# Performance work log

Hardware: AMD Instinct MI355X
Metric: run time of the kernel (lower is better)

The kernel has to match this reference:

```python
import jax, jax.numpy as jnp
import numpy as np

IMAGE_SIZE = (256, 704)
VOXEL_SIZE = (0.5, 0.5, 1.5)
N_VOXELS = (200, 200, 4)
VOXEL_CENTER = (0.0, 0.0, -1.7)
BN_EPS = 1e-5
B, N_CAM, C_IN, HF, WF, C_OUT = 2, 6, 256, 32, 88, 80


def _get_points():
    nx, ny, nz = N_VOXELS
    pts = jnp.stack(jnp.meshgrid(jnp.arange(nx), jnp.arange(ny), jnp.arange(nz), indexing='ij')).astype(jnp.float32)
    vs = jnp.asarray(VOXEL_SIZE, jnp.float32)
    origin = jnp.asarray(VOXEL_CENTER, jnp.float32) - jnp.asarray(N_VOXELS, jnp.float32) / 2.0 * vs
    pts = pts * vs.reshape(3, 1, 1, 1) + origin.reshape(3, 1, 1, 1)
    return pts.reshape(3, -1)  # [3, N], N = nx*ny*nz


def setup_inputs():
    key = jax.random.key(0)
    k0, k1 = jax.random.split(key)
    mlvl_feats = jax.random.normal(k0, (B, N_CAM, C_IN, HF, WF), jnp.float32)
    # realistic lidar2image = intrinsics @ extrinsics for 6 surround cameras
    H, W = IMAGE_SIZE
    K = np.eye(4, dtype=np.float32)
    K[0, 0], K[1, 1], K[0, 2], K[1, 2] = 350.0, 350.0, W / 2.0, H / 2.0
    l2i = np.zeros((B, N_CAM, 4, 4), np.float32)
    A = np.array([[0, -1, 0], [0, 0, -1], [1, 0, 0]], np.float32)  # lidar->camera axis remap
    for j in range(N_CAM):
        yaw = 2.0 * np.pi * j / N_CAM
        cz, sz = np.cos(yaw), np.sin(yaw)
        Rz = np.array([[cz, -sz, 0], [sz, cz, 0], [0, 0, 1]], np.float32)
        R = A @ Rz.T
        t = Rz @ np.array([1.0, 0.0, 1.5], np.float32)  # camera position in lidar frame
        E = np.eye(4, dtype=np.float32)
        E[:3, :3] = R
        E[:3, 3] = -R @ t
        l2i[:, j] = K @ E
    lidar2image = jnp.asarray(l2i)
    img_aug_matrix = jnp.tile(jnp.eye(4, dtype=jnp.float32), (B, N_CAM, 1, 1))
    lidar_aug_matrix = jnp.tile(jnp.eye(4, dtype=jnp.float32), (B, 1, 1))
    conv_w = jax.random.normal(k1, (C_OUT, C_IN), jnp.float32) * 0.05
    conv_b = jnp.zeros((C_OUT,), jnp.float32)
    bn_gamma = jnp.ones((C_OUT,), jnp.float32)
    bn_beta = jnp.zeros((C_OUT,), jnp.float32)
    bn_mean = jnp.zeros((C_OUT,), jnp.float32)
    bn_var = jnp.ones((C_OUT,), jnp.float32)
    return {"mlvl_feats": mlvl_feats, "lidar2image": lidar2image, "img_aug_matrix": img_aug_matrix,
            "lidar_aug_matrix": lidar_aug_matrix, "conv_w": conv_w, "conv_b": conv_b,
            "bn_gamma": bn_gamma, "bn_beta": bn_beta, "bn_mean": bn_mean, "bn_var": bn_var}


def _sample_volume(feat, l2i, iam, lam, pts):
    # feat: [n_cam, C, Hf, Wf]; l2i/iam: [n_cam,4,4]; lam: [4,4]; pts: [3,N]
    n_img, C, Hh, Ww = feat.shape
    stride = (IMAGE_SIZE[-1] + Ww - 1) // Ww  # ceil(image_W / feat_W)
    p = pts - lam[:3, 3:4]
    p = lam[:3, :3].T @ p  # inverse lidar aug
    iam_r = iam.at[:, :3, 3].set(0.0)  # img aug with translation zeroed
    proj = (iam_r @ l2i)[:, :3, :]  # [n_cam, 3, 4]
    ph = jnp.concatenate([p, jnp.ones((1, p.shape[1]), p.dtype)], axis=0)  # [4, N]
    p2i = jnp.einsum('nij,jk->nik', proj, ph)  # [n_cam, 3, N]
    Z = p2i[:, 2]
    u = p2i[:, 0] / Z + iam[:, 0, 3][:, None]
    v = p2i[:, 1] / Z + iam[:, 1, 3][:, None]
    u_fm = jnp.round(u / stride).astype(jnp.int32)
    v_fm = jnp.round(v / stride).astype(jnp.int32)
    valid = (u_fm >= 0) & (v_fm >= 0) & (u_fm < Ww) & (v_fm < Hh) & (Z > 0)
    uc = jnp.clip(u_fm, 0, Ww - 1)
    vc = jnp.clip(v_fm, 0, Hh - 1)
    vol = jnp.zeros((C, pts.shape[1]), feat.dtype)
    for j in range(n_img):  # fixed small camera count; later cameras overwrite, matching torch loop
        vol = jnp.where(valid[j][None, :], feat[j][:, vc[j], uc[j]], vol)
    return vol.reshape(C, *N_VOXELS).sum(axis=-1)  # sum over z -> [C, nx, ny]


def reference(mlvl_feats, lidar2image, img_aug_matrix, lidar_aug_matrix, conv_w, conv_b, bn_gamma, bn_beta, bn_mean, bn_var):
    pts = _get_points()
    bev = jax.vmap(_sample_volume, in_axes=(0, 0, 0, 0, None))(
        mlvl_feats, lidar2image, img_aug_matrix, lidar_aug_matrix, pts)  # [B, C, nx, ny]
    out = jnp.einsum('bcxy,oc->boxy', bev, conv_w) + conv_b[None, :, None, None]
    scale = (bn_gamma / jnp.sqrt(bn_var + BN_EPS))[None, :, None, None]
    out = (out - bn_mean[None, :, None, None]) * scale + bn_beta[None, :, None, None]
    return jnp.maximum(out, 0.0)
```

## Files before the change

### kernel.cpp

```cpp
#include <hip/hip_runtime.h>
#include <hip/hip_fp16.h>

#define BATCH 2
#define NCAM 6
#define CIN 256
#define COUT 80
#define HFEAT 32
#define WFEAT 88
#define HWF (HFEAT * WFEAT)
#define NXV 200
#define NYV 200
#define NZV 4
#define NPIX (NXV * NYV)
#define BN_EPS 1e-5f
#define CSPLIT 2
#define CHALF (COUT / CSPLIT)

#define NTILE 132
#define NTILE_PAD 136
#define FEATW_BLOCKS 544

#define WS_NEED ((size_t)BATCH * NCAM * HWF * COUT * 2)

__device__ __forceinline__ void compute_cam_mat(int b, int cam,
                                                const float* __restrict__ l2i,
                                                const float* __restrict__ iam,
                                                const float* __restrict__ lam,
                                                float* __restrict__ O ) {
    const float* L = lam + b * 16;
    const float* A = iam + (b * NCAM + cam) * 16;
    const float* P = l2i + (b * NCAM + cam) * 16;
    float Tl[3][4];
    #pragma unroll
    for (int i = 0; i < 3; i++) {
        #pragma unroll
        for (int j = 0; j < 3; j++) Tl[i][j] = L[j * 4 + i];
        Tl[i][3] = -(L[0 * 4 + i] * L[0 * 4 + 3] +
                     L[1 * 4 + i] * L[1 * 4 + 3] +
                     L[2 * 4 + i] * L[2 * 4 + 3]);
    }
    float Pm[3][4];
    #pragma unroll
    for (int i = 0; i < 3; i++)
        #pragma unroll
        for (int j = 0; j < 4; j++) {
            float s = 0.f;
            #pragma unroll
            for (int k = 0; k < 3; k++) s += A[i * 4 + k] * P[k * 4 + j];
            Pm[i][j] = s;
        }
    #pragma unroll
    for (int i = 0; i < 3; i++) {
        #pragma unroll
        for (int j = 0; j < 4; j++) {
            float s = (j == 3) ? Pm[i][3] : 0.f;
            #pragma unroll
            for (int k = 0; k < 3; k++) s += Pm[i][k] * Tl[k][j];
            O[i * 4 + j] = s;
        }
    }
    O[12] = A[0 * 4 + 3];
    O[13] = A[1 * 4 + 3];
    O[14] = 0.f;
    O[15] = 0.f;
}

__global__ __launch_bounds__(256) void k_featw(const float* __restrict__ feat,
                                               const float* __restrict__ W,
                                               __half* __restrict__ featW) {
    __shared__ __align__(16) float wl[CIN][20];
    const int id = blockIdx.x;
    const int r = id & 7;
    const int s = id >> 3;
    const int q = s % 17;
    const int og = s / 17;
    const int T = q * 8 + r;
    if (T >= NTILE) return;
    const int bc = T / 11;
    const int xt = T % 11;
    const int l = threadIdx.x;

    #pragma unroll
    for (int j = 0; j < 20; j++)
        wl[l][j] = W[(og * 20 + j) * CIN + l];
    __syncthreads();

    const int hw = xt * 256 + l;
    const float* f = feat + (size_t)bc * CIN * HWF + hw;

    float acc[20];
    #pragma unroll
    for (int j = 0; j < 20; j++) acc[j] = 0.f;

    float fbA[16], fbB[16];
    #pragma unroll
    for (int k = 0; k < 16; k++) fbA[k] = f[(size_t)k * HWF];

    #pragma unroll
    for (int cc = 0; cc < CIN; cc += 32) {
        #pragma unroll
        for (int k = 0; k < 16; k++) fbB[k] = f[(size_t)(cc + 16 + k) * HWF];
        #pragma unroll
        for (int k = 0; k < 16; k++) {
            float v = fbA[k];
            const float4* wr = reinterpret_cast<const float4*>(&wl[cc + k][0]);
            float4 w0 = wr[0], w1 = wr[1], w2 = wr[2], w3 = wr[3], w4 = wr[4];
            acc[0]  = fmaf(v, w0.x, acc[0]);   acc[1]  = fmaf(v, w0.y, acc[1]);
            acc[2]  = fmaf(v, w0.z, acc[2]);   acc[3]  = fmaf(v, w0.w, acc[3]);
            acc[4]  = fmaf(v, w1.x, acc[4]);   acc[5]  = fmaf(v, w1.y, acc[5]);
            acc[6]  = fmaf(v, w1.z, acc[6]);   acc[7]  = fmaf(v, w1.w, acc[7]);
            acc[8]  = fmaf(v, w2.x, acc[8]);   acc[9]  = fmaf(v, w2.y, acc[9]);
            acc[10] = fmaf(v, w2.z, acc[10]);  acc[11] = fmaf(v, w2.w, acc[11]);
            acc[12] = fmaf(v, w3.x, acc[12]);  acc[13] = fmaf(v, w3.y, acc[13]);
            acc[14] = fmaf(v, w3.z, acc[14]);  acc[15] = fmaf(v, w3.w, acc[15]);
            acc[16] = fmaf(v, w4.x, acc[16]);  acc[17] = fmaf(v, w4.y, acc[17]);
            acc[18] = fmaf(v, w4.z, acc[18]);  acc[19] = fmaf(v, w4.w, acc[19]);
        }
        if (cc + 32 < CIN) {
            #pragma unroll
            for (int k = 0; k < 16; k++) fbA[k] = f[(size_t)(cc + 32 + k) * HWF];
        }
        #pragma unroll
        for (int k = 0; k < 16; k++) {
            float v = fbB[k];
            const float4* wr = reinterpret_cast<const float4*>(&wl[cc + 16 + k][0]);
            float4 w0 = wr[0], w1 = wr[1], w2 = wr[2], w3 = wr[3], w4 = wr[4];
            acc[0]  = fmaf(v, w0.x, acc[0]);   acc[1]  = fmaf(v, w0.y, acc[1]);
            acc[2]  = fmaf(v, w0.z, acc[2]);   acc[3]  = fmaf(v, w0.w, acc[3]);
            acc[4]  = fmaf(v, w1.x, acc[4]);   acc[5]  = fmaf(v, w1.y, acc[5]);
            acc[6]  = fmaf(v, w1.z, acc[6]);   acc[7]  = fmaf(v, w1.w, acc[7]);
            acc[8]  = fmaf(v, w2.x, acc[8]);   acc[9]  = fmaf(v, w2.y, acc[9]);
            acc[10] = fmaf(v, w2.z, acc[10]);  acc[11] = fmaf(v, w2.w, acc[11]);
            acc[12] = fmaf(v, w3.x, acc[12]);  acc[13] = fmaf(v, w3.y, acc[13]);
            acc[14] = fmaf(v, w3.z, acc[14]);  acc[15] = fmaf(v, w3.w, acc[15]);
            acc[16] = fmaf(v, w4.x, acc[16]);  acc[17] = fmaf(v, w4.y, acc[17]);
            acc[18] = fmaf(v, w4.z, acc[18]);  acc[19] = fmaf(v, w4.w, acc[19]);
        }
    }

    __half2* dst = reinterpret_cast<__half2*>(
        featW + ((size_t)bc * HWF + hw) * COUT + og * 20);
    #pragma unroll
    for (int j = 0; j < 10; j++)
        dst[j] = __floats2half2_rn(acc[2 * j], acc[2 * j + 1]);
}

__device__ __forceinline__ int project_point(const float* __restrict__ M ,
                                             float x, float y, float z) {
    for (int cam = NCAM - 1; cam >= 0; --cam) {
        const float* m = M + cam * 16;
        float Z = m[8] * x + m[9] * y + m[10] * z + m[11];
        if (Z > 0.f) {
            float u = (m[0] * x + m[1] * y + m[2] * z + m[3]) / Z + m[12];
            float v = (m[4] * x + m[5] * y + m[6] * z + m[7]) / Z + m[13];
            float uf = rintf(u * 0.125f);
            float vf = rintf(v * 0.125f);
            if (uf >= 0.f && uf < (float)WFEAT && vf >= 0.f && vf < (float)HFEAT) {
                return cam * HWF + (int)vf * WFEAT + (int)uf;
            }
        }
    }
    return -1;
}

__device__ __forceinline__ void bn_precompute(const float* __restrict__ cb,
                                              const float* __restrict__ gamma,
                                              const float* __restrict__ beta,
                                              const float* __restrict__ mean,
                                              const float* __restrict__ var,
                                              float* __restrict__ s_scale,
                                              float* __restrict__ s_bias) {
    for (int o = threadIdx.x; o < COUT; o += 64) {
        float sc = gamma[o] / sqrtf(var[o] + BN_EPS);
        s_scale[o] = sc;
        s_bias[o] = (cb[o] - mean[o]) * sc + beta[o];
    }
}

__global__ __launch_bounds__(64) void k_bev(const __half* __restrict__ featW,
                                            const float* __restrict__ l2i,
                                            const float* __restrict__ iam,
                                            const float* __restrict__ lam,
                                            const float* __restrict__ cb,
                                            const float* __restrict__ gamma,
                                            const float* __restrict__ beta,
                                            const float* __restrict__ mean,
                                            const float* __restrict__ var,
                                            float* __restrict__ out) {
    __shared__ float smats[NCAM * 16];
    __shared__ float s_scale[COUT];
    __shared__ float s_bias[COUT];
    const int b = blockIdx.y;
    const int cs = blockIdx.z;
    if (threadIdx.x < NCAM)
        compute_cam_mat(b, threadIdx.x, l2i, iam, lam, smats + threadIdx.x * 16);
    bn_precompute(cb, gamma, beta, mean, var, s_scale, s_bias);
    __syncthreads();

    const int P = blockIdx.x * 64 + threadIdx.x;
    const int ix = P / NYV, iy = P % NYV;
    const float x = ix * 0.5f - 50.0f;
    const float y = iy * 0.5f - 50.0f;

    const __half* base = featW + (size_t)b * NCAM * HWF * COUT + cs * CHALF;
    const uint4* src[NZV];
    float vmask[NZV];
    #pragma unroll
    for (int iz = 0; iz < NZV; ++iz) {
        float z = iz * 1.5f - 4.7f;
        int off = project_point(smats, x, y, z);
        vmask[iz] = (off >= 0) ? 1.0f : 0.0f;
        src[iz] = reinterpret_cast<const uint4*>(
            base + (size_t)((off >= 0) ? off : 0) * COUT);
    }

    uint4 buf[NZV][5];
    #pragma unroll
    for (int iz = 0; iz < NZV; ++iz)
        #pragma unroll
        for (int i = 0; i < 5; i++) buf[iz][i] = src[iz][i];

    float acc[CHALF];
    #pragma unroll
    for (int k = 0; k < CHALF; k++) acc[k] = 0.f;
    #pragma unroll
    for (int iz = 0; iz < NZV; ++iz) {
        float m = vmask[iz];
        #pragma unroll
        for (int i = 0; i < 5; i++) {
            const __half2* h2 = reinterpret_cast<const __half2*>(&buf[iz][i]);
            #pragma unroll
            for (int k = 0; k < 4; k++) {
                float2 fv = __half22float2(h2[k]);
                acc[i * 8 + k * 2]     = fmaf(m, fv.x, acc[i * 8 + k * 2]);
                acc[i * 8 + k * 2 + 1] = fmaf(m, fv.y, acc[i * 8 + k * 2 + 1]);
            }
        }
    }

    float* op = out + ((size_t)b * COUT + cs * CHALF) * NPIX + P;
    #pragma unroll
    for (int k = 0; k < CHALF; k++) {
        int o = cs * CHALF + k;
        float val = fmaf(acc[k], s_scale[o], s_bias[o]);
        op[(size_t)k * NPIX] = fmaxf(val, 0.f);
    }
}

__global__ __launch_bounds__(64) void k_bev_fb(const float* __restrict__ feat,
                                               const float* __restrict__ l2i,
                                               const float* __restrict__ iam,
                                               const float* __restrict__ lam,
                                               const float* __restrict__ W,
                                               const float* __restrict__ cb,
                                               const float* __restrict__ gamma,
                                               const float* __restrict__ beta,
                                               const float* __restrict__ mean,
                                               const float* __restrict__ var,
                                               float* __restrict__ out) {
    __shared__ float smats[NCAM * 16];
    __shared__ float s_scale[COUT];
    __shared__ float s_bias[COUT];
    const int b = blockIdx.y;
    if (threadIdx.x < NCAM)
        compute_cam_mat(b, threadIdx.x, l2i, iam, lam, smats + threadIdx.x * 16);
    bn_precompute(cb, gamma, beta, mean, var, s_scale, s_bias);
    __syncthreads();

    const int P = blockIdx.x * 64 + threadIdx.x;
    const int ix = P / NYV, iy = P % NYV;
    const float x = ix * 0.5f - 50.0f;
    const float y = iy * 0.5f - 50.0f;

    float acc[COUT];
    #pragma unroll
    for (int o = 0; o < COUT; o++) acc[o] = 0.f;

    for (int iz = 0; iz < NZV; ++iz) {
        float z = iz * 1.5f - 4.7f;
        int off = project_point(smats, x, y, z);
        if (off >= 0) {
            const float* fp = feat + (size_t)b * NCAM * CIN * HWF +
                              (size_t)(off / HWF) * CIN * HWF + (off % HWF);
            for (int c = 0; c < CIN; c++) {
                float fv = fp[(size_t)c * HWF];
                #pragma unroll 8
                for (int o = 0; o < COUT; o++) acc[o] = fmaf(fv, W[o * CIN + c], acc[o]);
            }
        }
    }

    float* op = out + (size_t)b * COUT * NPIX + P;
    for (int o = 0; o < COUT; o++) {
        float val = fmaf(acc[o], s_scale[o], s_bias[o]);
        op[(size_t)o * NPIX] = fmaxf(val, 0.f);
    }
}

extern "C" void kernel_launch(void* const* d_in, const int* in_sizes, int n_in,
                              void* d_out, int out_size, void* d_ws, size_t ws_size,
                              hipStream_t stream) {
    const float* feat  = (const float*)d_in[0];
    const float* l2i   = (const float*)d_in[1];
    const float* iam   = (const float*)d_in[2];
    const float* lam   = (const float*)d_in[3];
    const float* W     = (const float*)d_in[4];
    const float* cb    = (const float*)d_in[5];
    const float* gamma = (const float*)d_in[6];
    const float* beta  = (const float*)d_in[7];
    const float* mean  = (const float*)d_in[8];
    const float* var   = (const float*)d_in[9];
    float* out = (float*)d_out;

    if (ws_size >= WS_NEED) {
        __half* featWp = (__half*)d_ws;
        k_featw<<<FEATW_BLOCKS, 256, 0, stream>>>(feat, W, featWp);
        k_bev<<<dim3(625, 2, CSPLIT), 64, 0, stream>>>(featWp, l2i, iam, lam, cb,
                                                       gamma, beta, mean, var, out);
    } else {
        k_bev_fb<<<dim3(625, 2), 64, 0, stream>>>(feat, l2i, iam, lam, W, cb, gamma,
                                                  beta, mean, var, out);
    }
}
```

Before: 134.0 us.

## Register-block four pixels per thread in feature-weight GEMM with 64-thread blocks

The projection GEMM kernel now runs 64 threads per block, and each thread computes four pixels (strided by 64) across 20 output channels. Each weight value read from shared memory is reused four times, cutting LDS traffic per FMA, and the feature prefetch depth is halved to 8 channels. The cost is many more live registers (80 accumulators plus 64 buffered features) and fewer waves per block, which may lower occupancy and latency hiding on the global loads.

New measurement: 292.2 us. 2.18x slower.

```diff
diff --git a/kernel.cpp b/kernel.cpp
--- a/kernel.cpp
+++ b/kernel.cpp
@@ -17,7 +17,6 @@
 #define CHALF (COUT / CSPLIT)
 
 #define NTILE 132
-#define NTILE_PAD 136
 #define FEATW_BLOCKS 544
 
 #define WS_NEED ((size_t)BATCH * NCAM * HWF * COUT * 2)
@@ -65,9 +64,9 @@
     O[15] = 0.f;
 }
 
-__global__ __launch_bounds__(256) void k_featw(const float* __restrict__ feat,
-                                               const float* __restrict__ W,
-                                               __half* __restrict__ featW) {
+__global__ __launch_bounds__(64, 2) void k_featw(const float* __restrict__ feat,
+                                                 const float* __restrict__ W,
+                                                 __half* __restrict__ featW) {
     __shared__ __align__(16) float wl[CIN][20];
     const int id = blockIdx.x;
     const int r = id & 7;
@@ -81,68 +80,81 @@
     const int l = threadIdx.x;
 
     #pragma unroll
+    for (int j = 0; j < 20; j++) {
+        #pragma unroll
+        for (int qq = 0; qq < 4; qq++) {
+            int c = qq * 64 + l;
+            wl[c][j] = W[(og * 20 + j) * CIN + c];
+        }
+    }
+    __syncthreads();
+
+    const int hw0 = xt * 256;
+    const float* f = feat + (size_t)bc * CIN * HWF + hw0 + l;
+
+    float acc[20][4];
+    #pragma unroll
     for (int j = 0; j < 20; j++)
-        wl[l][j] = W[(og * 20 + j) * CIN + l];
-    __syncthreads();
-
-    const int hw = xt * 256 + l;
-    const float* f = feat + (size_t)bc * CIN * HWF + hw;
-
-    float acc[20];
-    #pragma unroll
-    for (int j = 0; j < 20; j++) acc[j] = 0.f;
-
-    float fbA[16], fbB[16];
-    #pragma unroll
-    for (int k = 0; k < 16; k++) fbA[k] = f[(size_t)k * HWF];
-
-    #pragma unroll
-    for (int cc = 0; cc < CIN; cc += 32) {
-        #pragma unroll
-        for (int k = 0; k < 16; k++) fbB[k] = f[(size_t)(cc + 16 + k) * HWF];
-        #pragma unroll
-        for (int k = 0; k < 16; k++) {
-            float v = fbA[k];
+        #pragma unroll
+        for (int p = 0; p < 4; p++) acc[j][p] = 0.f;
+
+    float fbA[8][4], fbB[8][4];
+    #pragma unroll
+    for (int k = 0; k < 8; k++)
+        #pragma unroll
+        for (int p = 0; p < 4; p++)
+            fbA[k][p] = f[(size_t)k * HWF + p * 64];
+
+    #pragma unroll
+    for (int cc = 0; cc < CIN; cc += 16) {
+        #pragma unroll
+        for (int k = 0; k < 8; k++)
+            #pragma unroll
+            for (int p = 0; p < 4; p++)
+                fbB[k][p] = f[(size_t)(cc + 8 + k) * HWF + p * 64];
+        #pragma unroll
+        for (int k = 0; k < 8; k++) {
             const float4* wr = reinterpret_cast<const float4*>(&wl[cc + k][0]);
             float4 w0 = wr[0], w1 = wr[1], w2 = wr[2], w3 = wr[3], w4 = wr[4];
-            acc[0]  = fmaf(v, w0.x, acc[0]);   acc[1]  = fmaf(v, w0.y, acc[1]);
-            acc[2]  = fmaf(v, w0.z, acc[2]);   acc[3]  = fmaf(v, w0.w, acc[3]);
-            acc[4]  = fmaf(v, w1.x, acc[4]);   acc[5]  = fmaf(v, w1.y, acc[5]);
-            acc[6]  = fmaf(v, w1.z, acc[6]);   acc[7]  = fmaf(v, w1.w, acc[7]);
-            acc[8]  = fmaf(v, w2.x, acc[8]);   acc[9]  = fmaf(v, w2.y, acc[9]);
-            acc[10] = fmaf(v, w2.z, acc[10]);  acc[11] = fmaf(v, w2.w, acc[11]);
-            acc[12] = fmaf(v, w3.x, acc[12]);  acc[13] = fmaf(v, w3.y, acc[13]);
-            acc[14] = fmaf(v, w3.z, acc[14]);  acc[15] = fmaf(v, w3.w, acc[15]);
-            acc[16] = fmaf(v, w4.x, acc[16]);  acc[17] = fmaf(v, w4.y, acc[17]);
-            acc[18] = fmaf(v, w4.z, acc[18]);  acc[19] = fmaf(v, w4.w, acc[19]);
-        }
-        if (cc + 32 < CIN) {
-            #pragma unroll
-            for (int k = 0; k < 16; k++) fbA[k] = f[(size_t)(cc + 32 + k) * HWF];
-        }
-        #pragma unroll
-        for (int k = 0; k < 16; k++) {
-            float v = fbB[k];
-            const float4* wr = reinterpret_cast<const float4*>(&wl[cc + 16 + k][0]);
+            float wv[20] = {w0.x, w0.y, w0.z, w0.w, w1.x, w1.y, w1.z, w1.w,
+                            w2.x, w2.y, w2.z, w2.w, w3.x, w3.y, w3.z, w3.w,
+                            w4.x, w4.y, w4.z, w4.w};
+            #pragma unroll
+            for (int j = 0; j < 20; j++)
+                #pragma unroll
+                for (int p = 0; p < 4; p++)
+                    acc[j][p] = fmaf(fbA[k][p], wv[j], acc[j][p]);
+        }
+        if (cc + 16 < CIN) {
+            #pragma unroll
+            for (int k = 0; k < 8; k++)
+                #pragma unroll
+                for (int p = 0; p < 4; p++)
+                    fbA[k][p] = f[(size_t)(cc + 16 + k) * HWF + p * 64];
+        }
+        #pragma unroll
+        for (int k = 0; k < 8; k++) {
+            const float4* wr = reinterpret_cast<const float4*>(&wl[cc + 8 + k][0]);
             float4 w0 = wr[0], w1 = wr[1], w2 = wr[2], w3 = wr[3], w4 = wr[4];
-            acc[0]  = fmaf(v, w0.x, acc[0]);   acc[1]  = fmaf(v, w0.y, acc[1]);
-            acc[2]  = fmaf(v, w0.z, acc[2]);   acc[3]  = fmaf(v, w0.w, acc[3]);
-            acc[4]  = fmaf(v, w1.x, acc[4]);   acc[5]  = fmaf(v, w1.y, acc[5]);
-            acc[6]  = fmaf(v, w1.z, acc[6]);   acc[7]  = fmaf(v, w1.w, acc[7]);
-            acc[8]  = fmaf(v, w2.x, acc[8]);   acc[9]  = fmaf(v, w2.y, acc[9]);
-            acc[10] = fmaf(v, w2.z, acc[10]);  acc[11] = fmaf(v, w2.w, acc[11]);
-            acc[12] = fmaf(v, w3.x, acc[12]);  acc[13] = fmaf(v, w3.y, acc[13]);
-            acc[14] = fmaf(v, w3.z, acc[14]);  acc[15] = fmaf(v, w3.w, acc[15]);
-            acc[16] = fmaf(v, w4.x, acc[16]);  acc[17] = fmaf(v, w4.y, acc[17]);
-            acc[18] = fmaf(v, w4.z, acc[18]);  acc[19] = fmaf(v, w4.w, acc[19]);
-        }
-    }
-
-    __half2* dst = reinterpret_cast<__half2*>(
-        featW + ((size_t)bc * HWF + hw) * COUT + og * 20);
-    #pragma unroll
-    for (int j = 0; j < 10; j++)
-        dst[j] = __floats2half2_rn(acc[2 * j], acc[2 * j + 1]);
+            float wv[20] = {w0.x, w0.y, w0.z, w0.w, w1.x, w1.y, w1.z, w1.w,
+                            w2.x, w2.y, w2.z, w2.w, w3.x, w3.y, w3.z, w3.w,
+                            w4.x, w4.y, w4.z, w4.w};
+            #pragma unroll
+            for (int j = 0; j < 20; j++)
+                #pragma unroll
+                for (int p = 0; p < 4; p++)
+                    acc[j][p] = fmaf(fbB[k][p], wv[j], acc[j][p]);
+        }
+    }
+
+    #pragma unroll
+    for (int p = 0; p < 4; p++) {
+        __half2* dst = reinterpret_cast<__half2*>(
+            featW + ((size_t)bc * HWF + hw0 + p * 64 + l) * COUT + og * 20);
+        #pragma unroll
+        for (int j = 0; j < 10; j++)
+            dst[j] = __floats2half2_rn(acc[2 * j][p], acc[2 * j + 1][p]);
+    }
 }
 
 __device__ __forceinline__ int project_point(const float* __restrict__ M ,
@@ -314,7 +326,7 @@
 
     if (ws_size >= WS_NEED) {
         __half* featWp = (__half*)d_ws;
-        k_featw<<<FEATW_BLOCKS, 256, 0, stream>>>(feat, W, featWp);
+        k_featw<<<FEATW_BLOCKS, 64, 0, stream>>>(feat, W, featWp);
         k_bev<<<dim3(625, 2, CSPLIT), 64, 0, stream>>>(featWp, l2i, iam, lam, cb,
                                                        gamma, beta, mean, var, out);
     } else {
```
